# Optimization experiments

Hardware: AMD Instinct MI355X
Metric: run time of the kernel (lower is better)

The kernel has to match this reference:

```python
import jax, jax.numpy as jnp
import numpy as np

B, N, T = 64, 256, 512          # batch, num_objs, num_triples
DO, DP, H, DOUT = 512, 512, 512, 512


def setup_inputs() -> dict:
    key = jax.random.key(0)
    ks = jax.random.split(key, 12)

    def kaiming(k, shape):
        fan_in = shape[0]
        return jax.random.normal(k, shape, jnp.float32) * np.sqrt(2.0 / fan_in)

    return {
        "obj_vecs": jax.random.normal(ks[0], (B, N, DO), jnp.float32),
        "pred_vecs": jax.random.normal(ks[1], (B, T, DP), jnp.float32),
        "edges": jax.random.randint(ks[2], (B, T, 3), 0, N, jnp.int64),
        # net1: [2*DO+DP -> H -> 2*H+DOUT], ReLU after each Linear
        "n1_w1": kaiming(ks[3], (2 * DO + DP, H)),
        "n1_b1": jnp.zeros((H,), jnp.float32),
        "n1_w2": kaiming(ks[4], (H, 2 * H + DOUT)),
        "n1_b2": jnp.zeros((2 * H + DOUT,), jnp.float32),
        # net2: [H -> H -> DOUT], ReLU after each Linear
        "n2_w1": kaiming(ks[5], (H, H)),
        "n2_b1": jnp.zeros((H,), jnp.float32),
        "n2_w2": kaiming(ks[6], (H, DOUT)),
        "n2_b2": jnp.zeros((DOUT,), jnp.float32),
    }


def reference(obj_vecs, pred_vecs, edges,
              n1_w1, n1_b1, n1_w2, n1_b2,
              n2_w1, n2_b1, n2_w2, n2_b2):
    num_batch, num_objs, _ = obj_vecs.shape
    h_dim = n1_b1.shape[0]
    d_out = n2_w2.shape[1]

    s_idx = edges[:, :, 0]            # [B, T] subject node ids
    o_idx = edges[:, :, 2]            # [B, T] object node ids

    # gather subject/object vectors per triple
    cur_s = jnp.take_along_axis(obj_vecs, s_idx[:, :, None], axis=1)  # [B,T,DO]
    cur_o = jnp.take_along_axis(obj_vecs, o_idx[:, :, None], axis=1)  # [B,T,DO]
    cur_t = jnp.concatenate([cur_s, pred_vecs, cur_o], axis=-1)       # [B,T,2DO+DP]

    # net1 MLP (Linear+ReLU, Linear+ReLU)
    hid = jax.nn.relu(jnp.einsum('btd,dh->bth', cur_t, n1_w1) + n1_b1)
    new_t = jax.nn.relu(jnp.einsum('bth,hk->btk', hid, n1_w2) + n1_b2)

    new_s = new_t[:, :, :h_dim]
    new_p = new_t[:, :, h_dim:h_dim + d_out]
    new_o = new_t[:, :, h_dim + d_out:2 * h_dim + d_out]

    # scatter-add back to nodes, per batch element
    b_ix = jnp.arange(num_batch)[:, None]            # [B,1]
    pooled = jnp.zeros((num_batch, num_objs, h_dim), obj_vecs.dtype)
    pooled = pooled.at[b_ix, s_idx].add(new_s)
    pooled = pooled.at[b_ix, o_idx].add(new_o)

    # avg pooling: divide by per-node incidence count (clamped at 1)
    ones = jnp.ones(s_idx.shape, obj_vecs.dtype)
    counts = jnp.zeros((num_batch, num_objs), obj_vecs.dtype)
    counts = counts.at[b_ix, s_idx].add(ones)
    counts = counts.at[b_ix, o_idx].add(ones)
    counts = jnp.maximum(counts, 1.0)
    pooled = pooled / counts[:, :, None]

    # net2 MLP (Linear+ReLU, Linear+ReLU)
    h2 = jax.nn.relu(jnp.einsum('bnh,hk->bnk', pooled, n2_w1) + n2_b1)
    new_obj_vecs = jax.nn.relu(jnp.einsum('bnh,hd->bnd', h2, n2_w2) + n2_b2)

    return new_obj_vecs, new_p
```

## Files before the change

### kernel.cpp

```cpp
#include <hip/hip_runtime.h>

typedef __bf16 bf16;
typedef __attribute__((ext_vector_type(4))) __bf16 bf16x4;
typedef __attribute__((ext_vector_type(8))) __bf16 bf16x8;
typedef __attribute__((ext_vector_type(4))) float f32x4;

#define DEVINL __device__ __forceinline__

typedef __attribute__((address_space(1))) void gvoid_t;
typedef __attribute__((address_space(3))) void lvoid_t;

DEVINL void async_ld16(const void* g, void* l) {
    __builtin_amdgcn_global_load_lds((gvoid_t*)g, (lvoid_t*)l, 16, 0, 0);
}

template<int MODE>
__global__ __launch_bounds__(256, 2) void gemm_k(
    const bf16* __restrict__ A, const bf16* __restrict__ Bt,
    const float* __restrict__ bias, bf16* __restrict__ Dbf,
    float* __restrict__ Df, bf16* __restrict__ Dbf2,
    const int* __restrict__ edges, const bf16* __restrict__ obj,
    const bf16* __restrict__ pred, int K)
{
    const int tid = threadIdx.x;
    const int bn = blockIdx.x;
    const int bm = blockIdx.y;

    __shared__ __align__(16) bf16 ldsA[128 * 64];
    __shared__ __align__(16) bf16 ldsB[128 * 64];

    const int g_slot = tid & 7;
    const int row0 = tid >> 3;

    unsigned offS[4], offP[4], offO[4], offA[4], offB[4];
#pragma unroll
    for (int i = 0; i < 4; i++) {
        int r = row0 + 32 * i;
        int gr = bm * 128 + r;
        if (MODE == 0) {
            int b = gr >> 9;
            int s = edges[gr * 3 + 0] & 255;
            int o = edges[gr * 3 + 2] & 255;
            offS[i] = (unsigned)(b * 256 + s) * 512u;
            offP[i] = (unsigned)gr * 512u;
            offO[i] = (unsigned)(b * 256 + o) * 512u;
        } else {
            offA[i] = (unsigned)gr * (unsigned)K;
        }
        offB[i] = (unsigned)(bn * 128 + r) * (unsigned)K;
    }

    f32x4 acc[4][4];
    const f32x4 zero4 = {0.f, 0.f, 0.f, 0.f};
#pragma unroll
    for (int i = 0; i < 4; i++)
#pragma unroll
        for (int j = 0; j < 4; j++) acc[i][j] = zero4;

    const int wave = tid >> 6;
    const int lane = tid & 63;
    const int wr = (wave >> 1) * 64;
    const int wc = (wave & 1) * 64;
    const int lq = lane >> 4;
    const int lr = lane & 15;

    const int KT = K >> 6;
    for (int kt = 0; kt < KT; ++kt) {
        __syncthreads();
#pragma unroll
        for (int i = 0; i < 4; i++) {
            int r = row0 + 32 * i;
            int gsrc = g_slot ^ (r & 7);
            const bf16* gp;
            if (MODE == 0) {
                int region = kt >> 3;
                unsigned col = (unsigned)((kt & 7) * 64 + gsrc * 8);
                if (region == 0)      gp = obj + offS[i] + col;
                else if (region == 1) gp = pred + offP[i] + col;
                else                  gp = obj + offO[i] + col;
            } else {
                gp = A + offA[i] + (unsigned)(kt * 64 + gsrc * 8);
            }
            async_ld16(gp, ldsA + (tid + i * 256) * 8);
        }
#pragma unroll
        for (int i = 0; i < 4; i++) {
            int r = row0 + 32 * i;
            int gsrc = g_slot ^ (r & 7);
            async_ld16(Bt + offB[i] + (unsigned)(kt * 64 + gsrc * 8),
                       ldsB + (tid + i * 256) * 8);
        }
        __syncthreads();

#pragma unroll
        for (int ks = 0; ks < 2; ++ks) {
            bf16x8 af[4], bfr[4];
#pragma unroll
            for (int mi = 0; mi < 4; ++mi) {
                int r = wr + mi * 16 + lr;
                int g = (ks * 4 + lq) ^ (r & 7);
                af[mi] = *(const bf16x8*)(ldsA + (r * 8 + g) * 8);
            }
#pragma unroll
            for (int ni = 0; ni < 4; ++ni) {
                int r = wc + ni * 16 + lr;
                int g = (ks * 4 + lq) ^ (r & 7);
                bfr[ni] = *(const bf16x8*)(ldsB + (r * 8 + g) * 8);
            }
#pragma unroll
            for (int mi = 0; mi < 4; ++mi)
#pragma unroll
                for (int ni = 0; ni < 4; ++ni)
                    acc[mi][ni] = __builtin_amdgcn_mfma_f32_16x16x32_bf16(
                        bfr[ni], af[mi], acc[mi][ni], 0, 0, 0);
        }
    }

#pragma unroll
    for (int ni = 0; ni < 4; ++ni) {
        int col = bn * 128 + wc + ni * 16 + lq * 4;
        const f32x4 bv = *(const f32x4*)(bias + col);
#pragma unroll
        for (int mi = 0; mi < 4; ++mi) {
            int row = bm * 128 + wr + mi * 16 + lr;
            f32x4 v = acc[mi][ni];
            f32x4 x;
#pragma unroll
            for (int r = 0; r < 4; r++) {
                float t = v[r] + bv[r];
                x[r] = t > 0.f ? t : 0.f;
            }
            if (MODE == 1) {
                if (col < 512) {
                    bf16x4 o = { (bf16)x[0], (bf16)x[1], (bf16)x[2], (bf16)x[3] };
                    *(bf16x4*)(Dbf + row * 512 + col) = o;
                } else if (col < 1024) {
                    *(f32x4*)(Df + row * 512 + (col - 512)) = x;
                } else {
                    bf16x4 o = { (bf16)x[0], (bf16)x[1], (bf16)x[2], (bf16)x[3] };
                    *(bf16x4*)(Dbf2 + row * 512 + (col - 1024)) = o;
                }
            } else if (MODE == 3) {
                *(f32x4*)(Df + row * 512 + col) = x;
            } else {
                bf16x4 o = { (bf16)x[0], (bf16)x[1], (bf16)x[2], (bf16)x[3] };
                *(bf16x4*)(Dbf + row * 512 + col) = o;
            }
        }
    }
}

__global__ void cvt_k(const float4* __restrict__ s, bf16x4* __restrict__ d) {
    int i = blockIdx.x * 256 + threadIdx.x;
    float4 v = s[i];
    bf16x4 o = { (bf16)v.x, (bf16)v.y, (bf16)v.z, (bf16)v.w };
    d[i] = o;
}

__global__ void transpose_k(const float* __restrict__ src, bf16* __restrict__ dst,
                            int R, int C) {
    __shared__ float tile[32][33];
    int c0 = blockIdx.x * 32, r0 = blockIdx.y * 32;
    int tx = threadIdx.x, ty = threadIdx.y;
#pragma unroll
    for (int i = 0; i < 4; i++)
        tile[ty + i * 8][tx] = src[(size_t)(r0 + ty + i * 8) * C + c0 + tx];
    __syncthreads();
#pragma unroll
    for (int i = 0; i < 4; i++)
        dst[(size_t)(c0 + ty + i * 8) * R + r0 + tx] = (bf16)tile[tx][ty + i * 8];
}

__global__ void zero_i4_k(int4* __restrict__ p) {
    p[blockIdx.x * 256 + threadIdx.x] = make_int4(0, 0, 0, 0);
}

__global__ void count_k(const int* __restrict__ edges, int* __restrict__ counts) {
    int e = blockIdx.x * 256 + threadIdx.x;
    int b = e >> 9;
    atomicAdd(counts + b * 256 + (edges[e * 3 + 0] & 255), 1);
    atomicAdd(counts + b * 256 + (edges[e * 3 + 2] & 255), 1);
}

__global__ void scan_k(const int* __restrict__ counts, int* __restrict__ starts,
                       int* __restrict__ cursor) {
    __shared__ int s[256];
    int b = blockIdx.x, t = threadIdx.x;
    int idx = b * 256 + t;
    int c0 = counts[idx];
    s[t] = c0;
    __syncthreads();
#pragma unroll
    for (int off = 1; off < 256; off <<= 1) {
        int v = (t >= off) ? s[t - off] : 0;
        __syncthreads();
        s[t] += v;
        __syncthreads();
    }
    int excl = b * 1024 + s[t] - c0;
    starts[idx] = excl;
    cursor[idx] = excl;
}

__global__ void fill_k(const int* __restrict__ edges, int* __restrict__ cursor,
                       int* __restrict__ entries) {
    int e = blockIdx.x * 256 + threadIdx.x;
    int b = e >> 9;
    int s = edges[e * 3 + 0] & 255;
    int o = edges[e * 3 + 2] & 255;
    int ps = atomicAdd(cursor + b * 256 + s, 1);
    entries[ps] = e << 1;
    int po = atomicAdd(cursor + b * 256 + o, 1);
    entries[po] = (e << 1) | 1;
}

__global__ void pool_k(const int* __restrict__ entries, const int* __restrict__ starts,
                       const int* __restrict__ counts,
                       const bf16* __restrict__ new_s, const bf16* __restrict__ new_o,
                       bf16* __restrict__ out) {
    __shared__ int ent[1024];
    int idx = blockIdx.x;
    int t = threadIdx.x;
    int c = counts[idx], st = starts[idx];
    for (int j = t; j < c; j += 256) ent[j] = entries[st + j];
    __syncthreads();
    float a0 = 0.f, a1 = 0.f;
    for (int j = 0; j < c; ++j) {
        int v = ent[j];
        const bf16* rp = ((v & 1) ? new_o : new_s) + (unsigned)(v >> 1) * 512u;
        a0 += (float)rp[t];
        a1 += (float)rp[t + 256];
    }
    float inv = 1.f / (float)(c > 1 ? c : 1);
    out[(unsigned)idx * 512u + t]       = (bf16)(a0 * inv);
    out[(unsigned)idx * 512u + t + 256] = (bf16)(a1 * inv);
}

extern "C" void kernel_launch(void* const* d_in, const int* in_sizes, int n_in,
                              void* d_out, int out_size, void* d_ws, size_t ws_size,
                              hipStream_t stream) {
    const float* obj_f  = (const float*)d_in[0];
    const float* pred_f = (const float*)d_in[1];
    const int*   edges  = (const int*)d_in[2];
    const float* w1 = (const float*)d_in[3];
    const float* b1 = (const float*)d_in[4];
    const float* w2 = (const float*)d_in[5];
    const float* b2 = (const float*)d_in[6];
    const float* w3 = (const float*)d_in[7];
    const float* b3 = (const float*)d_in[8];
    const float* w4 = (const float*)d_in[9];
    const float* b4 = (const float*)d_in[10];

    char* ws = (char*)d_ws;
    bf16* obj_bf  = (bf16*)(ws + 0);
    bf16* pred_bf = (bf16*)(ws + 16777216);
    bf16* new_s   = (bf16*)(ws + 0);
    int* entries  = (int*)(ws + 33554432);
    int* counts   = (int*)(ws + 33816576);
    int* starts   = (int*)(ws + 33882112);
    int* cursor   = (int*)(ws + 33947648);
    bf16* w1t = (bf16*)(ws + 50331648);
    bf16* w2t = (bf16*)(ws + 51904512);
    bf16* w3t = (bf16*)(ws + 53477376);
    bf16* w4t = (bf16*)(ws + 54001664);
    bf16* hid = (bf16*)(ws + 54525952);
    bf16* pooled_bf = hid;
    bf16* h2  = (bf16*)(ws + 71303168);

    float* out_obj = (float*)d_out;
    float* out_p   = (float*)d_out + 8388608;
    bf16* new_o    = (bf16*)d_out;

    cvt_k<<<8192, 256, 0, stream>>>((const float4*)obj_f, (bf16x4*)obj_bf);
    cvt_k<<<16384, 256, 0, stream>>>((const float4*)pred_f, (bf16x4*)pred_bf);
    transpose_k<<<dim3(16, 48), dim3(32, 8), 0, stream>>>(w1, w1t, 1536, 512);
    transpose_k<<<dim3(48, 16), dim3(32, 8), 0, stream>>>(w2, w2t, 512, 1536);
    transpose_k<<<dim3(16, 16), dim3(32, 8), 0, stream>>>(w3, w3t, 512, 512);
    transpose_k<<<dim3(16, 16), dim3(32, 8), 0, stream>>>(w4, w4t, 512, 512);

    gemm_k<0><<<dim3(4, 256), 256, 0, stream>>>(
        nullptr, w1t, b1, hid, nullptr, nullptr, edges, obj_bf, pred_bf, 1536);

    zero_i4_k<<<16, 256, 0, stream>>>((int4*)counts);
    count_k<<<128, 256, 0, stream>>>(edges, counts);
    scan_k<<<64, 256, 0, stream>>>(counts, starts, cursor);
    fill_k<<<128, 256, 0, stream>>>(edges, cursor, entries);

    gemm_k<1><<<dim3(12, 256), 256, 0, stream>>>(
        hid, w2t, b2, new_s, out_p, new_o, nullptr, nullptr, nullptr, 512);

    pool_k<<<16384, 256, 0, stream>>>(entries, starts, counts, new_s, new_o, pooled_bf);

    gemm_k<2><<<dim3(4, 128), 256, 0, stream>>>(
        pooled_bf, w3t, b3, h2, nullptr, nullptr, nullptr, nullptr, nullptr, 512);
    gemm_k<3><<<dim3(4, 128), 256, 0, stream>>>(
        h2, w4t, b4, nullptr, out_obj, nullptr, nullptr, nullptr, nullptr, 512);
}
```

Before: 425.7 us.

## Merge prep kernels, build CSR in one LDS kernel, swizzle GEMM block order

```diff
diff --git a/kernel.cpp b/kernel.cpp
--- a/kernel.cpp
+++ b/kernel.cpp
@@ -14,7 +14,7 @@
     __builtin_amdgcn_global_load_lds((gvoid_t*)g, (lvoid_t*)l, 16, 0, 0);
 }
 
-template<int MODE>
+template<int MODE, int NBN>
 __global__ __launch_bounds__(256, 2) void gemm_k(
     const bf16* __restrict__ A, const bf16* __restrict__ Bt,
     const float* __restrict__ bias, bf16* __restrict__ Dbf,
@@ -23,8 +23,9 @@
     const bf16* __restrict__ pred, int K)
 {
     const int tid = threadIdx.x;
-    const int bn = blockIdx.x;
-    const int bm = blockIdx.y;
+    const int id = blockIdx.x;
+    const int bn = (id >> 3) % NBN;
+    const int bm = (id & 7) + 8 * ((id >> 3) / NBN);
 
     __shared__ __align__(16) bf16 ldsA[128 * 64];
     __shared__ __align__(16) bf16 ldsB[128 * 64];
@@ -150,17 +151,33 @@
     }
 }
 
-__global__ void cvt_k(const float4* __restrict__ s, bf16x4* __restrict__ d) {
+__global__ void cvt2_k(const float4* __restrict__ o, const float4* __restrict__ p,
+                       bf16x4* __restrict__ ob, bf16x4* __restrict__ pb) {
     int i = blockIdx.x * 256 + threadIdx.x;
-    float4 v = s[i];
-    bf16x4 o = { (bf16)v.x, (bf16)v.y, (bf16)v.z, (bf16)v.w };
-    d[i] = o;
-}
-
-__global__ void transpose_k(const float* __restrict__ src, bf16* __restrict__ dst,
-                            int R, int C) {
+    if (i < 2097152) {
+        float4 v = o[i];
+        bf16x4 r = { (bf16)v.x, (bf16)v.y, (bf16)v.z, (bf16)v.w };
+        ob[i] = r;
+    } else {
+        int j = i - 2097152;
+        float4 v = p[j];
+        bf16x4 r = { (bf16)v.x, (bf16)v.y, (bf16)v.z, (bf16)v.w };
+        pb[j] = r;
+    }
+}
+
+__global__ void transpose4_k(const float* __restrict__ w1, bf16* __restrict__ w1t,
+                             const float* __restrict__ w2, bf16* __restrict__ w2t,
+                             const float* __restrict__ w3, bf16* __restrict__ w3t,
+                             const float* __restrict__ w4, bf16* __restrict__ w4t) {
     __shared__ float tile[32][33];
-    int c0 = blockIdx.x * 32, r0 = blockIdx.y * 32;
+    int id = blockIdx.x;
+    const float* src; bf16* dst; int R, C, bx, by;
+    if (id < 768)       { src = w1; dst = w1t; R = 1536; C = 512;  bx = id % 16; by = id / 16; }
+    else if (id < 1536) { id -= 768;  src = w2; dst = w2t; R = 512; C = 1536; bx = id % 48; by = id / 48; }
+    else if (id < 1792) { id -= 1536; src = w3; dst = w3t; R = 512; C = 512;  bx = id % 16; by = id / 16; }
+    else                { id -= 1792; src = w4; dst = w4t; R = 512; C = 512;  bx = id % 16; by = id / 16; }
+    int c0 = bx * 32, r0 = by * 32;
     int tx = threadIdx.x, ty = threadIdx.y;
 #pragma unroll
     for (int i = 0; i < 4; i++)
@@ -171,23 +188,22 @@
         dst[(size_t)(c0 + ty + i * 8) * R + r0 + tx] = (bf16)tile[tx][ty + i * 8];
 }
 
-__global__ void zero_i4_k(int4* __restrict__ p) {
-    p[blockIdx.x * 256 + threadIdx.x] = make_int4(0, 0, 0, 0);
-}
-
-__global__ void count_k(const int* __restrict__ edges, int* __restrict__ counts) {
-    int e = blockIdx.x * 256 + threadIdx.x;
-    int b = e >> 9;
-    atomicAdd(counts + b * 256 + (edges[e * 3 + 0] & 255), 1);
-    atomicAdd(counts + b * 256 + (edges[e * 3 + 2] & 255), 1);
-}
-
-__global__ void scan_k(const int* __restrict__ counts, int* __restrict__ starts,
-                       int* __restrict__ cursor) {
+__global__ void csr_k(const int* __restrict__ edges, int* __restrict__ counts_g,
+                      int* __restrict__ starts_g, int* __restrict__ entries) {
+    __shared__ int cnt[256];
     __shared__ int s[256];
+    __shared__ int cur[256];
     int b = blockIdx.x, t = threadIdx.x;
-    int idx = b * 256 + t;
-    int c0 = counts[idx];
+    cnt[t] = 0;
+    __syncthreads();
+#pragma unroll
+    for (int e = 0; e < 2; e++) {
+        int row = b * 512 + t + e * 256;
+        atomicAdd(&cnt[edges[row * 3 + 0] & 255], 1);
+        atomicAdd(&cnt[edges[row * 3 + 2] & 255], 1);
+    }
+    __syncthreads();
+    int c0 = cnt[t];
     s[t] = c0;
     __syncthreads();
 #pragma unroll
@@ -197,21 +213,21 @@
         s[t] += v;
         __syncthreads();
     }
-    int excl = b * 1024 + s[t] - c0;
-    starts[idx] = excl;
-    cursor[idx] = excl;
-}
-
-__global__ void fill_k(const int* __restrict__ edges, int* __restrict__ cursor,
-                       int* __restrict__ entries) {
-    int e = blockIdx.x * 256 + threadIdx.x;
-    int b = e >> 9;
-    int s = edges[e * 3 + 0] & 255;
-    int o = edges[e * 3 + 2] & 255;
-    int ps = atomicAdd(cursor + b * 256 + s, 1);
-    entries[ps] = e << 1;
-    int po = atomicAdd(cursor + b * 256 + o, 1);
-    entries[po] = (e << 1) | 1;
+    int excl = s[t] - c0;
+    counts_g[b * 256 + t] = c0;
+    starts_g[b * 256 + t] = b * 1024 + excl;
+    cur[t] = excl;
+    __syncthreads();
+#pragma unroll
+    for (int e = 0; e < 2; e++) {
+        int row = b * 512 + t + e * 256;
+        int si = edges[row * 3 + 0] & 255;
+        int oi = edges[row * 3 + 2] & 255;
+        int ps = atomicAdd(&cur[si], 1);
+        entries[b * 1024 + ps] = row << 1;
+        int po = atomicAdd(&cur[oi], 1);
+        entries[b * 1024 + po] = (row << 1) | 1;
+    }
 }
 
 __global__ void pool_k(const int* __restrict__ entries, const int* __restrict__ starts,
@@ -258,7 +274,6 @@
     int* entries  = (int*)(ws + 33554432);
     int* counts   = (int*)(ws + 33816576);
     int* starts   = (int*)(ws + 33882112);
-    int* cursor   = (int*)(ws + 33947648);
     bf16* w1t = (bf16*)(ws + 50331648);
     bf16* w2t = (bf16*)(ws + 51904512);
     bf16* w3t = (bf16*)(ws + 53477376);
@@ -271,28 +286,22 @@
     float* out_p   = (float*)d_out + 8388608;
     bf16* new_o    = (bf16*)d_out;
 
-    cvt_k<<<8192, 256, 0, stream>>>((const float4*)obj_f, (bf16x4*)obj_bf);
-    cvt_k<<<16384, 256, 0, stream>>>((const float4*)pred_f, (bf16x4*)pred_bf);
-    transpose_k<<<dim3(16, 48), dim3(32, 8), 0, stream>>>(w1, w1t, 1536, 512);
-    transpose_k<<<dim3(48, 16), dim3(32, 8), 0, stream>>>(w2, w2t, 512, 1536);
-    transpose_k<<<dim3(16, 16), dim3(32, 8), 0, stream>>>(w3, w3t, 512, 512);
-    transpose_k<<<dim3(16, 16), dim3(32, 8), 0, stream>>>(w4, w4t, 512, 512);
-
-    gemm_k<0><<<dim3(4, 256), 256, 0, stream>>>(
+    cvt2_k<<<24576, 256, 0, stream>>>((const float4*)obj_f, (const float4*)pred_f,
+                                      (bf16x4*)obj_bf, (bf16x4*)pred_bf);
+    transpose4_k<<<2048, dim3(32, 8), 0, stream>>>(w1, w1t, w2, w2t, w3, w3t, w4, w4t);
+
+    gemm_k<0, 4><<<1024, 256, 0, stream>>>(
         nullptr, w1t, b1, hid, nullptr, nullptr, edges, obj_bf, pred_bf, 1536);
 
-    zero_i4_k<<<16, 256, 0, stream>>>((int4*)counts);
-    count_k<<<128, 256, 0, stream>>>(edges, counts);
-    scan_k<<<64, 256, 0, stream>>>(counts, starts, cursor);
-    fill_k<<<128, 256, 0, stream>>>(edges, cursor, entries);
-
-    gemm_k<1><<<dim3(12, 256), 256, 0, stream>>>(
+    csr_k<<<64, 256, 0, stream>>>(edges, counts, starts, entries);
+
+    gemm_k<1, 12><<<3072, 256, 0, stream>>>(
         hid, w2t, b2, new_s, out_p, new_o, nullptr, nullptr, nullptr, 512);
 
     pool_k<<<16384, 256, 0, stream>>>(entries, starts, counts, new_s, new_o, pooled_bf);
 
-    gemm_k<2><<<dim3(4, 128), 256, 0, stream>>>(
+    gemm_k<2, 4><<<512, 256, 0, stream>>>(
         pooled_bf, w3t, b3, h2, nullptr, nullptr, nullptr, nullptr, nullptr, 512);
-    gemm_k<3><<<dim3(4, 128), 256, 0, stream>>>(
+    gemm_k<3, 4><<<512, 256, 0, stream>>>(
         h2, w4t, b4, nullptr, out_obj, nullptr, nullptr, nullptr, nullptr, 512);
 }
```

Result: faster. 389.3 us (-8.5%).
